# Kernel optimization log

Hardware: AMD Instinct MI355X
Metric: run time of the kernel (lower is better)

The kernel has to match this reference:

```python
import jax, jax.numpy as jnp
import numpy as np

WS = 8      # window size
NH = 8      # num heads
DIM = 192


def _rel_coords_table(ws):
    c = np.arange(-(ws - 1), ws, dtype=np.float32)
    t = np.stack(np.meshgrid(c, c, indexing='ij'), axis=-1)  # (2ws-1, 2ws-1, 2)
    t = t / (ws - 1) * 8.0
    t = np.sign(t) * np.log2(np.abs(t) + 1.0) / np.log2(8.0)
    return jnp.asarray(t.reshape(-1, 2))


def _rel_pos_index(ws):
    coords = np.stack(np.meshgrid(np.arange(ws), np.arange(ws), indexing='ij'))  # (2,ws,ws)
    cf = coords.reshape(2, -1)
    rel = (cf[:, :, None] - cf[:, None, :]).transpose(1, 2, 0).astype(np.int64)  # (N,N,2)
    rel[..., 0] += ws - 1
    rel[..., 1] += ws - 1
    rel[..., 0] *= 2 * ws - 1
    return jnp.asarray(rel.sum(-1))  # (N,N)


_RCT = _rel_coords_table(WS)   # (225, 2)
_RPI = _rel_pos_index(WS)      # (64, 64)


def setup_inputs() -> dict:
    key = jax.random.key(0)
    ks = jax.random.split(key, 6)
    B, C, H, W = 4, DIM, 256, 256
    return {
        'x': jax.random.normal(ks[0], (B, C, H, W), dtype=jnp.float32),
        'img_alpha': jnp.ones((B, 1, H, W), dtype=jnp.float32),
        'qkv_w': jax.random.normal(ks[1], (3 * C, C), dtype=jnp.float32) * 0.02,
        'q_bias': jnp.zeros((C,), dtype=jnp.float32),
        'v_bias': jnp.zeros((C,), dtype=jnp.float32),
        'logit_scale': jnp.full((NH, 1, 1), np.log(10.0), dtype=jnp.float32),
        'cpb_w1': jax.random.normal(ks[2], (2, 512), dtype=jnp.float32) * 0.02,
        'cpb_b1': jnp.zeros((512,), dtype=jnp.float32),
        'cpb_w2': jax.random.normal(ks[3], (512, NH), dtype=jnp.float32) * 0.02,
        'proj_w': jax.random.normal(ks[4], (C, C), dtype=jnp.float32) * 0.02,
        'proj_b': jnp.zeros((C,), dtype=jnp.float32),
    }


def _forward(x, qkv_w, q_bias, v_bias, logit_scale, cpb_w1, cpb_b1, cpb_w2, proj_w, proj_b):
    B, C, H, W = x.shape
    ws, nh = WS, NH
    hd = C // nh
    # window partition: (B,C,H,W) -> (B*nW, N, C) with N = ws*ws
    xw = (x.transpose(0, 2, 3, 1)
           .reshape(B, H // ws, ws, W // ws, ws, C)
           .transpose(0, 1, 3, 2, 4, 5)
           .reshape(-1, ws * ws, C))
    Bw, N, _ = xw.shape
    # qkv with bias = [q_bias, 0, v_bias]
    qkv_b = jnp.concatenate([q_bias, jnp.zeros_like(v_bias), v_bias])
    qkv = (xw @ qkv_w.T + qkv_b).reshape(Bw, N, 3, nh, hd).transpose(2, 0, 3, 1, 4)
    q, k, v = qkv[0], qkv[1], qkv[2]  # (Bw, nh, N, hd)
    # cosine attention with clamped learnable logit scale
    qn = q / jnp.maximum(jnp.linalg.norm(q, axis=-1, keepdims=True), 1e-12)
    kn = k / jnp.maximum(jnp.linalg.norm(k, axis=-1, keepdims=True), 1e-12)
    scale = jnp.exp(jnp.minimum(logit_scale, jnp.log(jnp.float32(100.0))))  # (nh,1,1)
    attn = jnp.einsum('bhnd,bhmd->bhnm', qn, kn) * scale
    # relative position bias from small MLP + gather
    table = jax.nn.relu(_RCT @ cpb_w1 + cpb_b1) @ cpb_w2        # (225, nh)
    bias = table[_RPI.reshape(-1)].reshape(N, N, nh).transpose(2, 0, 1)  # (nh,N,N)
    bias = 16.0 * jax.nn.sigmoid(bias)
    attn = jax.nn.softmax(attn + bias[None], axis=-1)
    out = jnp.einsum('bhnm,bhmd->bhnd', attn, v).transpose(0, 2, 1, 3).reshape(Bw, N, C)
    out = out @ proj_w.T + proj_b
    # window reverse -> (B,C,H,W)
    out = (out.reshape(B, H // ws, W // ws, ws, ws, C)
              .transpose(0, 1, 3, 2, 4, 5)
              .reshape(B, H, W, C)
              .transpose(0, 3, 1, 2))
    return x + out  # residual (shortcut)


def reference(x, img_alpha, qkv_w, q_bias, v_bias, logit_scale,
              cpb_w1, cpb_b1, cpb_w2, proj_w, proj_b):
    # shift_size == 0: img_alpha only rides along through partition and is sliced off;
    # with all-ones alpha the zero-window removal is a no-op, so it does not affect output.
    del img_alpha
    return _forward(x, qkv_w, q_bias, v_bias, logit_scale,
                    cpb_w1, cpb_b1, cpb_w2, proj_w, proj_b)
```

## Files before the change

kernel.cpp:

```cpp
#include <hip/hip_runtime.h>

typedef unsigned short u16;
typedef __attribute__((ext_vector_type(8))) short bf16x8;
typedef __attribute__((ext_vector_type(4))) float f32x4;

#define C_    192
#define HW_   65536

__device__ inline u16 f2bf(float f) {
  union { float f; unsigned u; } x; x.f = f;
  unsigned r = x.u + 0x7FFFu + ((x.u >> 16) & 1u);
  return (u16)(r >> 16);
}
__device__ inline float bf2f(u16 s) {
  union { unsigned u; float f; } x; x.u = ((unsigned)s) << 16;
  return x.f;
}

__global__ void k_convert(const float* __restrict__ qkv_w, const float* __restrict__ proj_w,
                          const float* __restrict__ q_bias, const float* __restrict__ v_bias,
                          u16* __restrict__ wq, u16* __restrict__ wp, float* __restrict__ qkvb) {
  int i = blockIdx.x * 256 + threadIdx.x;
  if (i < 110592) wq[i] = f2bf(qkv_w[i]);
  else if (i < 147456) wp[i - 110592] = f2bf(proj_w[i - 110592]);
  else if (i < 148032) {
    int j = i - 147456;
    qkvb[j] = (j < 192) ? q_bias[j] : ((j < 384) ? 0.f : v_bias[j - 384]);
  }
}

__global__ void k_table(const float* __restrict__ w1, const float* __restrict__ b1,
                        const float* __restrict__ w2, float* __restrict__ table) {
  int row = blockIdx.x;
  int tid = threadIdx.x;
  int a = row / 15, b = row % 15;
  float va = (float)(a - 7) * (8.0f / 7.0f);
  float vb = (float)(b - 7) * (8.0f / 7.0f);
  float c0 = copysignf(log2f(fabsf(va) + 1.0f) * (1.0f / 3.0f), va);
  float c1 = copysignf(log2f(fabsf(vb) + 1.0f) * (1.0f / 3.0f), vb);
  float acc[8];
#pragma unroll
  for (int o = 0; o < 8; ++o) acc[o] = 0.f;
  for (int k = tid; k < 512; k += 256) {
    float h = fmaxf(c0 * w1[k] + c1 * w1[512 + k] + b1[k], 0.f);
#pragma unroll
    for (int o = 0; o < 8; ++o) acc[o] += h * w2[k * 8 + o];
  }
  __shared__ float part[4][8];
  int wave = tid >> 6;
#pragma unroll
  for (int o = 0; o < 8; ++o) {
    float v = acc[o];
    v += __shfl_xor(v, 1, 64);  v += __shfl_xor(v, 2, 64);
    v += __shfl_xor(v, 4, 64);  v += __shfl_xor(v, 8, 64);
    v += __shfl_xor(v, 16, 64); v += __shfl_xor(v, 32, 64);
    acc[o] = v;
  }
  if ((tid & 63) == 0)
#pragma unroll
    for (int o = 0; o < 8; ++o) part[wave][o] = acc[o];
  __syncthreads();
  if (tid < 8)
    table[row * 8 + tid] = part[0][tid] + part[1][tid] + part[2][tid] + part[3][tid];
}

__global__ void k_biasfill(const float* __restrict__ table, float* __restrict__ bias3) {
  int p = blockIdx.x * 256 + threadIdx.x;
  int h = p >> 12, t = (p >> 6) & 63, g = (p >> 4) & 3, u = p & 15;
  int nt = u >> 2, r = u & 3;
  int s = nt * 16 + g * 4 + r;
  int idx = ((t >> 3) - (s >> 3) + 7) * 15 + ((t & 7) - (s & 7) + 7);
  float v = table[idx * 8 + h];
  bias3[p] = 16.0f / (1.0f + __expf(-v));
}

__device__ __forceinline__ void attn_window(
    u16* __restrict__ R0, u16* __restrict__ Sw, float* __restrict__ ikw,
    const u16* __restrict__ wq, const float* __restrict__ qkvb,
    const float* __restrict__ bias3,
    int h, int g, int li, float scaleh,
    const bf16x8* qw0, const bf16x8* qw1) {
  bf16x8 z8 = {0, 0, 0, 0, 0, 0, 0, 0};
  f32x4 zf = {0.f, 0.f, 0.f, 0.f};
  float iqr[4];
  bf16x8 qf[4], kf[4];

  {
    f32x4 cb0 = *(const f32x4*)(qkvb + h * 24 + g * 4);
    f32x4 cb1 = *(const f32x4*)(qkvb + h * 24 + 16 + g * 4);
#pragma unroll
    for (int tb = 0; tb < 4; ++tb) {
      int t = tb * 16 + li;
      bf16x8 xf[6];
#pragma unroll
      for (int ks = 0; ks < 6; ++ks)
        xf[ks] = *(const bf16x8*)&R0[t * 200 + ks * 32 + g * 8];
      f32x4 a0 = zf, a1 = zf;
#pragma unroll
      for (int ks = 0; ks < 6; ++ks) {
        a0 = __builtin_amdgcn_mfma_f32_16x16x32_bf16(qw0[ks], xf[ks], a0, 0, 0, 0);
        a1 = __builtin_amdgcn_mfma_f32_16x16x32_bf16(qw1[ks], xf[ks], a1, 0, 0, 0);
      }
      float p = 0.f;
#pragma unroll
      for (int r = 0; r < 4; ++r) { a0[r] += cb0[r]; p += a0[r] * a0[r]; }
      if (g < 2) {
#pragma unroll
        for (int r = 0; r < 4; ++r) { a1[r] += cb1[r]; p += a1[r] * a1[r]; }
      }
      p += __shfl_xor(p, 16, 64);
      p += __shfl_xor(p, 32, 64);
      iqr[tb] = __builtin_amdgcn_rsqf(fmaxf(p, 1e-24f)) * scaleh;
      uint2 pk;
      pk.x = f2bf(a0[0]) | ((unsigned)f2bf(a0[1]) << 16);
      pk.y = f2bf(a0[2]) | ((unsigned)f2bf(a0[3]) << 16);
      *(uint2*)&Sw[t * 24 + g * 4] = pk;
      if (g < 2) {
        pk.x = f2bf(a1[0]) | ((unsigned)f2bf(a1[1]) << 16);
        pk.y = f2bf(a1[2]) | ((unsigned)f2bf(a1[3]) << 16);
        *(uint2*)&Sw[t * 24 + 16 + g * 4] = pk;
      }
    }
  }

  bf16x8 kw0[6], kw1[6];
  {
    const u16* wr0 = wq + (size_t)(192 + h * 24 + li) * 192 + g * 8;
    const u16* wr1 = wq + (size_t)(192 + h * 24 + 16 + (li & 7)) * 192 + g * 8;
#pragma unroll
    for (int ks = 0; ks < 6; ++ks) {
      kw0[ks] = *(const bf16x8*)(wr0 + ks * 32);
      kw1[ks] = *(const bf16x8*)(wr1 + ks * 32);
    }
  }
#pragma unroll
  for (int tb = 0; tb < 4; ++tb)
    qf[tb] = (g < 3) ? *(const bf16x8*)&Sw[(tb * 16 + li) * 24 + g * 8] : z8;

  {
    f32x4 cb0 = *(const f32x4*)(qkvb + 192 + h * 24 + g * 4);
    f32x4 cb1 = *(const f32x4*)(qkvb + 192 + h * 24 + 16 + g * 4);
#pragma unroll
    for (int nt = 0; nt < 4; ++nt) {
      int t = nt * 16 + li;
      bf16x8 xf[6];
#pragma unroll
      for (int ks = 0; ks < 6; ++ks)
        xf[ks] = *(const bf16x8*)&R0[t * 200 + ks * 32 + g * 8];
      f32x4 a0 = zf, a1 = zf;
#pragma unroll
      for (int ks = 0; ks < 6; ++ks) {
        a0 = __builtin_amdgcn_mfma_f32_16x16x32_bf16(kw0[ks], xf[ks], a0, 0, 0, 0);
        a1 = __builtin_amdgcn_mfma_f32_16x16x32_bf16(kw1[ks], xf[ks], a1, 0, 0, 0);
      }
      float p = 0.f;
#pragma unroll
      for (int r = 0; r < 4; ++r) { a0[r] += cb0[r]; p += a0[r] * a0[r]; }
      if (g < 2) {
#pragma unroll
        for (int r = 0; r < 4; ++r) { a1[r] += cb1[r]; p += a1[r] * a1[r]; }
      }
      p += __shfl_xor(p, 16, 64);
      p += __shfl_xor(p, 32, 64);
      float ik = __builtin_amdgcn_rsqf(fmaxf(p, 1e-24f));
      if (g == 0) ikw[h * 64 + t] = ik;
      uint2 pk;
      pk.x = f2bf(a0[0]) | ((unsigned)f2bf(a0[1]) << 16);
      pk.y = f2bf(a0[2]) | ((unsigned)f2bf(a0[3]) << 16);
      *(uint2*)&Sw[t * 24 + g * 4] = pk;
      if (g < 2) {
        pk.x = f2bf(a1[0]) | ((unsigned)f2bf(a1[1]) << 16);
        pk.y = f2bf(a1[2]) | ((unsigned)f2bf(a1[3]) << 16);
        *(uint2*)&Sw[t * 24 + 16 + g * 4] = pk;
      }
    }
  }

  bf16x8 vw0[6], vw1[6];
  {
    const u16* wr0 = wq + (size_t)(384 + h * 24 + li) * 192 + g * 8;
    const u16* wr1 = wq + (size_t)(384 + h * 24 + 16 + (li & 7)) * 192 + g * 8;
#pragma unroll
    for (int ks = 0; ks < 6; ++ks) {
      vw0[ks] = *(const bf16x8*)(wr0 + ks * 32);
      vw1[ks] = *(const bf16x8*)(wr1 + ks * 32);
    }
  }
#pragma unroll
  for (int nt = 0; nt < 4; ++nt)
    kf[nt] = (g < 3) ? *(const bf16x8*)&Sw[(nt * 16 + li) * 24 + g * 8] : z8;

  {
    float vb0 = qkvb[384 + h * 24 + li];
    float vb1 = qkvb[384 + h * 24 + 16 + (li & 7)];
#pragma unroll
    for (int tb = 0; tb < 4; ++tb) {
      int t = tb * 16 + li;
      bf16x8 xf[6];
#pragma unroll
      for (int ks = 0; ks < 6; ++ks)
        xf[ks] = *(const bf16x8*)&R0[t * 200 + ks * 32 + g * 8];
      f32x4 a0 = zf, a1 = zf;
#pragma unroll
      for (int ks = 0; ks < 6; ++ks) {
        a0 = __builtin_amdgcn_mfma_f32_16x16x32_bf16(xf[ks], vw0[ks], a0, 0, 0, 0);
        a1 = __builtin_amdgcn_mfma_f32_16x16x32_bf16(xf[ks], vw1[ks], a1, 0, 0, 0);
      }
      uint2 pk;
      pk.x = f2bf(a0[0] + vb0) | ((unsigned)f2bf(a0[1] + vb0) << 16);
      pk.y = f2bf(a0[2] + vb0) | ((unsigned)f2bf(a0[3] + vb0) << 16);
      *(uint2*)&Sw[li * 64 + tb * 16 + g * 4] = pk;
      if (li < 8) {
        pk.x = f2bf(a1[0] + vb1) | ((unsigned)f2bf(a1[1] + vb1) << 16);
        pk.y = f2bf(a1[2] + vb1) | ((unsigned)f2bf(a1[3] + vb1) << 16);
        *(uint2*)&Sw[(16 + li) * 64 + tb * 16 + g * 4] = pk;
      }
    }
  }
  bf16x8 vf0[2], vf1[2];
#pragma unroll
  for (int ks = 0; ks < 2; ++ks) {
    vf0[ks] = *(const bf16x8*)&Sw[li * 64 + ks * 32 + g * 8];
    vf1[ks] = (li < 8) ? *(const bf16x8*)&Sw[(16 + li) * 64 + ks * 32 + g * 8] : z8;
  }

  f32x4 bx[2][4];
  {
    const float* bp0 = bias3 + ((h * 64 + li) << 6) + (g << 4);
#pragma unroll
    for (int nt = 0; nt < 4; ++nt) bx[0][nt] = *(const f32x4*)(bp0 + (nt << 2));
  }
#pragma unroll
  for (int tb = 0; tb < 4; ++tb) {
    if (tb < 3) {
      const float* bpn = bias3 + ((h * 64 + (tb + 1) * 16 + li) << 6) + (g << 4);
#pragma unroll
      for (int nt = 0; nt < 4; ++nt) bx[(tb + 1) & 1][nt] = *(const f32x4*)(bpn + (nt << 2));
    }
    f32x4 s4[4];
#pragma unroll
    for (int nt = 0; nt < 4; ++nt)
      s4[nt] = __builtin_amdgcn_mfma_f32_16x16x32_bf16(kf[nt], qf[tb], zf, 0, 0, 0);
    float iq = iqr[tb];
#pragma unroll
    for (int nt = 0; nt < 4; ++nt) {
      f32x4 ik4 = *(const f32x4*)&ikw[h * 64 + nt * 16 + g * 4];
#pragma unroll
      for (int r = 0; r < 4; ++r)
        s4[nt][r] = s4[nt][r] * iq * ik4[r] + bx[tb & 1][nt][r];
    }
    float m = s4[0][0];
#pragma unroll
    for (int nt = 0; nt < 4; ++nt)
#pragma unroll
      for (int r = 0; r < 4; ++r) m = fmaxf(m, s4[nt][r]);
    m = fmaxf(m, __shfl_xor(m, 16, 64));
    m = fmaxf(m, __shfl_xor(m, 32, 64));
    float sum = 0.f;
#pragma unroll
    for (int nt = 0; nt < 4; ++nt)
#pragma unroll
      for (int r = 0; r < 4; ++r) { float e = __expf(s4[nt][r] - m); s4[nt][r] = e; sum += e; }
    sum += __shfl_xor(sum, 16, 64);
    sum += __shfl_xor(sum, 32, 64);
    float is = __builtin_amdgcn_rcpf(sum);
#pragma unroll
    for (int nt = 0; nt < 4; ++nt) {
      uint2 pk;
      pk.x = f2bf(s4[nt][0]) | ((unsigned)f2bf(s4[nt][1]) << 16);
      pk.y = f2bf(s4[nt][2]) | ((unsigned)f2bf(s4[nt][3]) << 16);
      *(uint2*)&Sw[li * 72 + nt * 16 + g * 4] = pk;
    }
    f32x4 o0 = zf, o1 = zf;
#pragma unroll
    for (int ks = 0; ks < 2; ++ks) {
      bf16x8 pf = *(const bf16x8*)&Sw[li * 72 + ks * 32 + g * 8];
      o0 = __builtin_amdgcn_mfma_f32_16x16x32_bf16(vf0[ks], pf, o0, 0, 0, 0);
      o1 = __builtin_amdgcn_mfma_f32_16x16x32_bf16(vf1[ks], pf, o1, 0, 0, 0);
    }
    int t = tb * 16 + li;
    {
      uint2 pk;
      pk.x = f2bf(o0[0] * is) | ((unsigned)f2bf(o0[1] * is) << 16);
      pk.y = f2bf(o0[2] * is) | ((unsigned)f2bf(o0[3] * is) << 16);
      *(uint2*)&R0[t * 200 + h * 24 + g * 4] = pk;
    }
    if (g < 2) {
      uint2 pk;
      pk.x = f2bf(o1[0] * is) | ((unsigned)f2bf(o1[1] * is) << 16);
      pk.y = f2bf(o1[2] * is) | ((unsigned)f2bf(o1[3] * is) << 16);
      *(uint2*)&R0[t * 200 + h * 24 + 16 + g * 4] = pk;
    }
  }
}

__global__ __launch_bounds__(512, 2)
void k_main(const float* __restrict__ x,
            const float* __restrict__ ls, const float* __restrict__ proj_b,
            const u16* __restrict__ wq, const u16* __restrict__ wp,
            const float* __restrict__ qkvb, const float* __restrict__ bias3,
            float* __restrict__ out) {
  __shared__ u16 smem[38912];
  u16* R0A = smem;
  u16* R0B = smem + 12800;
  u16* Sc  = smem + 25600;
  float* ikw = (float*)(smem + 37888);

  int tid  = threadIdx.x;
  int h = tid >> 6, lane = tid & 63, g = lane >> 4, li = lane & 15;
  int tt = h & 3, half = h >> 2;
  int bid = blockIdx.x;
  int b = bid >> 9, rem = bid & 511, wy = rem >> 4, wxp = rem & 15;
  const float* xb = x + (size_t)b * C_ * HW_;
  int baseA = (wy * 8) * 256 + wxp * 16;
  f32x4 zf = {0.f, 0.f, 0.f, 0.f};

  bf16x8 qwA0[6], qwA1[6];
  {
    const u16* wr0 = wq + (size_t)(h * 24 + li) * 192 + g * 8;
    const u16* wr1 = wq + (size_t)(h * 24 + 16 + (li & 7)) * 192 + g * 8;
#pragma unroll
    for (int ks = 0; ks < 6; ++ks) {
      qwA0[ks] = *(const bf16x8*)(wr0 + ks * 32);
      qwA1[ks] = *(const bf16x8*)(wr1 + ks * 32);
    }
  }

#pragma unroll
  for (int it = 0; it < 12; ++it) {
    int i4 = tid + it * 512;
    int c = i4 >> 5, r5 = i4 & 31;
    int ty = r5 >> 2, jq = (r5 & 3) * 4;
    float4 v = *(const float4*)(xb + c * HW_ + baseA + ty * 256 + jq);
    u16* Rw = (jq < 8) ? R0A : R0B;
    int t0 = ty * 8 + (jq & 7);
    Rw[(t0 + 0) * 200 + c] = f2bf(v.x);
    Rw[(t0 + 1) * 200 + c] = f2bf(v.y);
    Rw[(t0 + 2) * 200 + c] = f2bf(v.z);
    Rw[(t0 + 3) * 200 + c] = f2bf(v.w);
  }
  __syncthreads();

  u16* Sw = Sc + h * 1536;
  float scaleh = __expf(fminf(ls[h], 4.6051702f));

  attn_window(R0A, Sw, ikw, wq, qkvb, bias3, h, g, li, scaleh, qwA0, qwA1);

  bf16x8 qwB0[6], qwB1[6];
  {
    const u16* wr0 = wq + (size_t)(h * 24 + li) * 192 + g * 8;
    const u16* wr1 = wq + (size_t)(h * 24 + 16 + (li & 7)) * 192 + g * 8;
#pragma unroll
    for (int ks = 0; ks < 6; ++ks) {
      qwB0[ks] = *(const bf16x8*)(wr0 + ks * 32);
      qwB1[ks] = *(const bf16x8*)(wr1 + ks * 32);
    }
  }
  attn_window(R0B, Sw, ikw, wq, qkvb, bias3, h, g, li, scaleh, qwB0, qwB1);
  __syncthreads();

  bf16x8 afA[6], afB[6];
#pragma unroll
  for (int ks = 0; ks < 6; ++ks) {
    afA[ks] = *(const bf16x8*)&R0A[(tt * 16 + li) * 200 + ks * 32 + g * 8];
    afB[ks] = *(const bf16x8*)&R0B[(tt * 16 + li) * 200 + ks * 32 + g * 8];
  }
  __syncthreads();

  u16* obufA = Sc;
  u16* obufB = smem;
#pragma unroll
  for (int it = 0; it < 6; ++it) {
    int ct = half * 96 + it * 16;
    const u16* wr = wp + (size_t)(ct + li) * 192 + g * 8;
    bf16x8 w6[6];
#pragma unroll
    for (int ks = 0; ks < 6; ++ks) w6[ks] = *(const bf16x8*)(wr + ks * 32);
    f32x4 aA0 = zf, aA1 = zf, aB0 = zf, aB1 = zf;
#pragma unroll
    for (int ks = 0; ks < 3; ++ks) {
      aA0 = __builtin_amdgcn_mfma_f32_16x16x32_bf16(afA[ks], w6[ks], aA0, 0, 0, 0);
      aA1 = __builtin_amdgcn_mfma_f32_16x16x32_bf16(afA[ks + 3], w6[ks + 3], aA1, 0, 0, 0);
      aB0 = __builtin_amdgcn_mfma_f32_16x16x32_bf16(afB[ks], w6[ks], aB0, 0, 0, 0);
      aB1 = __builtin_amdgcn_mfma_f32_16x16x32_bf16(afB[ks + 3], w6[ks + 3], aB1, 0, 0, 0);
    }
    float pb = proj_b[ct + li];
    uint2 pk;
    pk.x = f2bf(aA0[0] + aA1[0] + pb) | ((unsigned)f2bf(aA0[1] + aA1[1] + pb) << 16);
    pk.y = f2bf(aA0[2] + aA1[2] + pb) | ((unsigned)f2bf(aA0[3] + aA1[3] + pb) << 16);
    *(uint2*)&obufA[(ct + li) * 68 + tt * 16 + g * 4] = pk;
    pk.x = f2bf(aB0[0] + aB1[0] + pb) | ((unsigned)f2bf(aB0[1] + aB1[1] + pb) << 16);
    pk.y = f2bf(aB0[2] + aB1[2] + pb) | ((unsigned)f2bf(aB0[3] + aB1[3] + pb) << 16);
    *(uint2*)&obufB[(ct + li) * 68 + tt * 16 + g * 4] = pk;
  }
  __syncthreads();

  float* ob = out + (size_t)b * C_ * HW_;
#pragma unroll
  for (int bt = 0; bt < 2; ++bt) {
    float4 xv[6];
    uint2 ov[6];
#pragma unroll
    for (int it = 0; it < 6; ++it) {
      int i4 = tid + (bt * 6 + it) * 512;
      int c = i4 >> 5, r5 = i4 & 31;
      int ty = r5 >> 2, jq = (r5 & 3) * 4;
      xv[it] = *(const float4*)(xb + c * HW_ + baseA + ty * 256 + jq);
    }
#pragma unroll
    for (int it = 0; it < 6; ++it) {
      int i4 = tid + (bt * 6 + it) * 512;
      int c = i4 >> 5, r5 = i4 & 31;
      int ty = r5 >> 2, jq = (r5 & 3) * 4;
      const u16* obw = (jq < 8) ? obufA : obufB;
      ov[it] = *(const uint2*)&obw[c * 68 + ty * 8 + (jq & 7)];
    }
#pragma unroll
    for (int it = 0; it < 6; ++it) {
      int i4 = tid + (bt * 6 + it) * 512;
      int c = i4 >> 5, r5 = i4 & 31;
      int ty = r5 >> 2, jq = (r5 & 3) * 4;
      float4 r;
      r.x = xv[it].x + bf2f((u16)(ov[it].x & 0xFFFFu));
      r.y = xv[it].y + bf2f((u16)(ov[it].x >> 16));
      r.z = xv[it].z + bf2f((u16)(ov[it].y & 0xFFFFu));
      r.w = xv[it].w + bf2f((u16)(ov[it].y >> 16));
      *(float4*)(ob + c * HW_ + baseA + ty * 256 + jq) = r;
    }
  }
}

extern "C" void kernel_launch(void* const* d_in, const int* in_sizes, int n_in,
                              void* d_out, int out_size, void* d_ws, size_t ws_size,
                              hipStream_t stream) {
  const float* x      = (const float*)d_in[0];
  const float* qkv_w  = (const float*)d_in[2];
  const float* q_bias = (const float*)d_in[3];
  const float* v_bias = (const float*)d_in[4];
  const float* ls     = (const float*)d_in[5];
  const float* w1     = (const float*)d_in[6];
  const float* b1     = (const float*)d_in[7];
  const float* w2     = (const float*)d_in[8];
  const float* proj_w = (const float*)d_in[9];
  const float* proj_b = (const float*)d_in[10];

  u16*   wq    = (u16*)d_ws;
  u16*   wpv   = wq + 110592;
  float* qkvb  = (float*)((char*)d_ws + 294912);
  float* bias3 = (float*)((char*)d_ws + 297216);
  float* table = (float*)((char*)d_ws + 428288);
  float* out   = (float*)d_out;

  hipLaunchKernelGGL(k_convert, dim3(579), dim3(256), 0, stream,
                     qkv_w, proj_w, q_bias, v_bias, wq, wpv, qkvb);
  hipLaunchKernelGGL(k_table, dim3(225), dim3(256), 0, stream, w1, b1, w2, table);
  hipLaunchKernelGGL(k_biasfill, dim3(128), dim3(256), 0, stream, table, bias3);
  hipLaunchKernelGGL(k_main, dim3(2048), dim3(512), 0, stream,
                     x, ls, proj_b, wq, wpv, qkvb, bias3, out);
}
```

Baseline: 424.8 us.

## Process two window pairs per block and pad V scratch stride

Each block now loops over two adjacent window pairs, which halves the grid to 1024 blocks and loads the Q weight fragments into registers once per block instead of twice per pair. The V transpose scratch row stride grows from 64 to 72 elements, likely to cut LDS bank conflicts. The key-norm buffer becomes a separate per-head slice outside the scratch area. The aim is less redundant weight loading and block launch overhead, at the cost of fewer blocks to spread across CUs and slightly more LDS per block.

```diff
diff --git a/kernel.cpp b/kernel.cpp
--- a/kernel.cpp
+++ b/kernel.cpp
@@ -163,7 +163,7 @@
       p += __shfl_xor(p, 16, 64);
       p += __shfl_xor(p, 32, 64);
       float ik = __builtin_amdgcn_rsqf(fmaxf(p, 1e-24f));
-      if (g == 0) ikw[h * 64 + t] = ik;
+      if (g == 0) ikw[t] = ik;
       uint2 pk;
       pk.x = f2bf(a0[0]) | ((unsigned)f2bf(a0[1]) << 16);
       pk.y = f2bf(a0[2]) | ((unsigned)f2bf(a0[3]) << 16);
@@ -209,19 +209,19 @@
       uint2 pk;
       pk.x = f2bf(a0[0] + vb0) | ((unsigned)f2bf(a0[1] + vb0) << 16);
       pk.y = f2bf(a0[2] + vb0) | ((unsigned)f2bf(a0[3] + vb0) << 16);
-      *(uint2*)&Sw[li * 64 + tb * 16 + g * 4] = pk;
+      *(uint2*)&Sw[li * 72 + tb * 16 + g * 4] = pk;
       if (li < 8) {
         pk.x = f2bf(a1[0] + vb1) | ((unsigned)f2bf(a1[1] + vb1) << 16);
         pk.y = f2bf(a1[2] + vb1) | ((unsigned)f2bf(a1[3] + vb1) << 16);
-        *(uint2*)&Sw[(16 + li) * 64 + tb * 16 + g * 4] = pk;
+        *(uint2*)&Sw[(16 + li) * 72 + tb * 16 + g * 4] = pk;
       }
     }
   }
   bf16x8 vf0[2], vf1[2];
 #pragma unroll
   for (int ks = 0; ks < 2; ++ks) {
-    vf0[ks] = *(const bf16x8*)&Sw[li * 64 + ks * 32 + g * 8];
-    vf1[ks] = (li < 8) ? *(const bf16x8*)&Sw[(16 + li) * 64 + ks * 32 + g * 8] : z8;
+    vf0[ks] = *(const bf16x8*)&Sw[li * 72 + ks * 32 + g * 8];
+    vf1[ks] = (li < 8) ? *(const bf16x8*)&Sw[(16 + li) * 72 + ks * 32 + g * 8] : z8;
   }
 
   f32x4 bx[2][4];
@@ -244,7 +244,7 @@
     float iq = iqr[tb];
 #pragma unroll
     for (int nt = 0; nt < 4; ++nt) {
-      f32x4 ik4 = *(const f32x4*)&ikw[h * 64 + nt * 16 + g * 4];
+      f32x4 ik4 = *(const f32x4*)&ikw[nt * 16 + g * 4];
 #pragma unroll
       for (int r = 0; r < 4; ++r)
         s4[nt][r] = s4[nt][r] * iq * ik4[r] + bx[tb & 1][nt][r];
@@ -300,133 +300,127 @@
             const u16* __restrict__ wq, const u16* __restrict__ wp,
             const float* __restrict__ qkvb, const float* __restrict__ bias3,
             float* __restrict__ out) {
-  __shared__ u16 smem[38912];
+  __shared__ u16 smem[40448];
   u16* R0A = smem;
   u16* R0B = smem + 12800;
   u16* Sc  = smem + 25600;
-  float* ikw = (float*)(smem + 37888);
+  float* ikwb = (float*)(smem + 39424);
 
   int tid  = threadIdx.x;
   int h = tid >> 6, lane = tid & 63, g = lane >> 4, li = lane & 15;
   int tt = h & 3, half = h >> 2;
   int bid = blockIdx.x;
-  int b = bid >> 9, rem = bid & 511, wy = rem >> 4, wxp = rem & 15;
+  int b = bid >> 8, rem = bid & 255, wy = rem >> 3, wxq = rem & 7;
   const float* xb = x + (size_t)b * C_ * HW_;
-  int baseA = (wy * 8) * 256 + wxp * 16;
   f32x4 zf = {0.f, 0.f, 0.f, 0.f};
 
-  bf16x8 qwA0[6], qwA1[6];
+  u16* Sw = Sc + h * 1728;
+  float* ikw = ikwb + h * 64;
+  float scaleh = __expf(fminf(ls[h], 4.6051702f));
+
+  bf16x8 qw0[6], qw1[6];
   {
     const u16* wr0 = wq + (size_t)(h * 24 + li) * 192 + g * 8;
     const u16* wr1 = wq + (size_t)(h * 24 + 16 + (li & 7)) * 192 + g * 8;
 #pragma unroll
     for (int ks = 0; ks < 6; ++ks) {
-      qwA0[ks] = *(const bf16x8*)(wr0 + ks * 32);
-      qwA1[ks] = *(const bf16x8*)(wr1 + ks * 32);
-    }
-  }
-
-#pragma unroll
-  for (int it = 0; it < 12; ++it) {
-    int i4 = tid + it * 512;
-    int c = i4 >> 5, r5 = i4 & 31;
-    int ty = r5 >> 2, jq = (r5 & 3) * 4;
-    float4 v = *(const float4*)(xb + c * HW_ + baseA + ty * 256 + jq);
-    u16* Rw = (jq < 8) ? R0A : R0B;
-    int t0 = ty * 8 + (jq & 7);
-    Rw[(t0 + 0) * 200 + c] = f2bf(v.x);
-    Rw[(t0 + 1) * 200 + c] = f2bf(v.y);
-    Rw[(t0 + 2) * 200 + c] = f2bf(v.z);
-    Rw[(t0 + 3) * 200 + c] = f2bf(v.w);
-  }
-  __syncthreads();
-
-  u16* Sw = Sc + h * 1536;
-  float scaleh = __expf(fminf(ls[h], 4.6051702f));
-
-  attn_window(R0A, Sw, ikw, wq, qkvb, bias3, h, g, li, scaleh, qwA0, qwA1);
-
-  bf16x8 qwB0[6], qwB1[6];
-  {
-    const u16* wr0 = wq + (size_t)(h * 24 + li) * 192 + g * 8;
-    const u16* wr1 = wq + (size_t)(h * 24 + 16 + (li & 7)) * 192 + g * 8;
-#pragma unroll
-    for (int ks = 0; ks < 6; ++ks) {
-      qwB0[ks] = *(const bf16x8*)(wr0 + ks * 32);
-      qwB1[ks] = *(const bf16x8*)(wr1 + ks * 32);
-    }
-  }
-  attn_window(R0B, Sw, ikw, wq, qkvb, bias3, h, g, li, scaleh, qwB0, qwB1);
-  __syncthreads();
-
-  bf16x8 afA[6], afB[6];
-#pragma unroll
-  for (int ks = 0; ks < 6; ++ks) {
-    afA[ks] = *(const bf16x8*)&R0A[(tt * 16 + li) * 200 + ks * 32 + g * 8];
-    afB[ks] = *(const bf16x8*)&R0B[(tt * 16 + li) * 200 + ks * 32 + g * 8];
-  }
-  __syncthreads();
-
-  u16* obufA = Sc;
-  u16* obufB = smem;
-#pragma unroll
-  for (int it = 0; it < 6; ++it) {
-    int ct = half * 96 + it * 16;
-    const u16* wr = wp + (size_t)(ct + li) * 192 + g * 8;
-    bf16x8 w6[6];
-#pragma unroll
-    for (int ks = 0; ks < 6; ++ks) w6[ks] = *(const bf16x8*)(wr + ks * 32);
-    f32x4 aA0 = zf, aA1 = zf, aB0 = zf, aB1 = zf;
-#pragma unroll
-    for (int ks = 0; ks < 3; ++ks) {
-      aA0 = __builtin_amdgcn_mfma_f32_16x16x32_bf16(afA[ks], w6[ks], aA0, 0, 0, 0);
-      aA1 = __builtin_amdgcn_mfma_f32_16x16x32_bf16(afA[ks + 3], w6[ks + 3], aA1, 0, 0, 0);
-      aB0 = __builtin_amdgcn_mfma_f32_16x16x32_bf16(afB[ks], w6[ks], aB0, 0, 0, 0);
-      aB1 = __builtin_amdgcn_mfma_f32_16x16x32_bf16(afB[ks + 3], w6[ks + 3], aB1, 0, 0, 0);
-    }
-    float pb = proj_b[ct + li];
-    uint2 pk;
-    pk.x = f2bf(aA0[0] + aA1[0] + pb) | ((unsigned)f2bf(aA0[1] + aA1[1] + pb) << 16);
-    pk.y = f2bf(aA0[2] + aA1[2] + pb) | ((unsigned)f2bf(aA0[3] + aA1[3] + pb) << 16);
-    *(uint2*)&obufA[(ct + li) * 68 + tt * 16 + g * 4] = pk;
-    pk.x = f2bf(aB0[0] + aB1[0] + pb) | ((unsigned)f2bf(aB0[1] + aB1[1] + pb) << 16);
-    pk.y = f2bf(aB0[2] + aB1[2] + pb) | ((unsigned)f2bf(aB0[3] + aB1[3] + pb) << 16);
-    *(uint2*)&obufB[(ct + li) * 68 + tt * 16 + g * 4] = pk;
-  }
-  __syncthreads();
-
-  float* ob = out + (size_t)b * C_ * HW_;
-#pragma unroll
-  for (int bt = 0; bt < 2; ++bt) {
-    float4 xv[6];
-    uint2 ov[6];
-#pragma unroll
-    for (int it = 0; it < 6; ++it) {
-      int i4 = tid + (bt * 6 + it) * 512;
+      qw0[ks] = *(const bf16x8*)(wr0 + ks * 32);
+      qw1[ks] = *(const bf16x8*)(wr1 + ks * 32);
+    }
+  }
+
+  for (int pair = 0; pair < 2; ++pair) {
+    int baseA = (wy * 8) * 256 + wxq * 32 + pair * 16;
+
+#pragma unroll
+    for (int it = 0; it < 12; ++it) {
+      int i4 = tid + it * 512;
       int c = i4 >> 5, r5 = i4 & 31;
       int ty = r5 >> 2, jq = (r5 & 3) * 4;
-      xv[it] = *(const float4*)(xb + c * HW_ + baseA + ty * 256 + jq);
-    }
+      float4 v = *(const float4*)(xb + c * HW_ + baseA + ty * 256 + jq);
+      u16* Rw = (jq < 8) ? R0A : R0B;
+      int t0 = ty * 8 + (jq & 7);
+      Rw[(t0 + 0) * 200 + c] = f2bf(v.x);
+      Rw[(t0 + 1) * 200 + c] = f2bf(v.y);
+      Rw[(t0 + 2) * 200 + c] = f2bf(v.z);
+      Rw[(t0 + 3) * 200 + c] = f2bf(v.w);
+    }
+    __syncthreads();
+
+    attn_window(R0A, Sw, ikw, wq, qkvb, bias3, h, g, li, scaleh, qw0, qw1);
+    attn_window(R0B, Sw, ikw, wq, qkvb, bias3, h, g, li, scaleh, qw0, qw1);
+    __syncthreads();
+
+    bf16x8 afA[6], afB[6];
+#pragma unroll
+    for (int ks = 0; ks < 6; ++ks) {
+      afA[ks] = *(const bf16x8*)&R0A[(tt * 16 + li) * 200 + ks * 32 + g * 8];
+      afB[ks] = *(const bf16x8*)&R0B[(tt * 16 + li) * 200 + ks * 32 + g * 8];
+    }
+    __syncthreads();
+
+    u16* obufA = Sc;
+    u16* obufB = smem;
 #pragma unroll
     for (int it = 0; it < 6; ++it) {
-      int i4 = tid + (bt * 6 + it) * 512;
-      int c = i4 >> 5, r5 = i4 & 31;
-      int ty = r5 >> 2, jq = (r5 & 3) * 4;
-      const u16* obw = (jq < 8) ? obufA : obufB;
-      ov[it] = *(const uint2*)&obw[c * 68 + ty * 8 + (jq & 7)];
-    }
-#pragma unroll
-    for (int it = 0; it < 6; ++it) {
-      int i4 = tid + (bt * 6 + it) * 512;
-      int c = i4 >> 5, r5 = i4 & 31;
-      int ty = r5 >> 2, jq = (r5 & 3) * 4;
-      float4 r;
-      r.x = xv[it].x + bf2f((u16)(ov[it].x & 0xFFFFu));
-      r.y = xv[it].y + bf2f((u16)(ov[it].x >> 16));
-      r.z = xv[it].z + bf2f((u16)(ov[it].y & 0xFFFFu));
-      r.w = xv[it].w + bf2f((u16)(ov[it].y >> 16));
-      *(float4*)(ob + c * HW_ + baseA + ty * 256 + jq) = r;
-    }
+      int ct = half * 96 + it * 16;
+      const u16* wr = wp + (size_t)(ct + li) * 192 + g * 8;
+      bf16x8 w6[6];
+#pragma unroll
+      for (int ks = 0; ks < 6; ++ks) w6[ks] = *(const bf16x8*)(wr + ks * 32);
+      f32x4 aA0 = zf, aA1 = zf, aB0 = zf, aB1 = zf;
+#pragma unroll
+      for (int ks = 0; ks < 3; ++ks) {
+        aA0 = __builtin_amdgcn_mfma_f32_16x16x32_bf16(afA[ks], w6[ks], aA0, 0, 0, 0);
+        aA1 = __builtin_amdgcn_mfma_f32_16x16x32_bf16(afA[ks + 3], w6[ks + 3], aA1, 0, 0, 0);
+        aB0 = __builtin_amdgcn_mfma_f32_16x16x32_bf16(afB[ks], w6[ks], aB0, 0, 0, 0);
+        aB1 = __builtin_amdgcn_mfma_f32_16x16x32_bf16(afB[ks + 3], w6[ks + 3], aB1, 0, 0, 0);
+      }
+      float pb = proj_b[ct + li];
+      uint2 pk;
+      pk.x = f2bf(aA0[0] + aA1[0] + pb) | ((unsigned)f2bf(aA0[1] + aA1[1] + pb) << 16);
+      pk.y = f2bf(aA0[2] + aA1[2] + pb) | ((unsigned)f2bf(aA0[3] + aA1[3] + pb) << 16);
+      *(uint2*)&obufA[(ct + li) * 68 + tt * 16 + g * 4] = pk;
+      pk.x = f2bf(aB0[0] + aB1[0] + pb) | ((unsigned)f2bf(aB0[1] + aB1[1] + pb) << 16);
+      pk.y = f2bf(aB0[2] + aB1[2] + pb) | ((unsigned)f2bf(aB0[3] + aB1[3] + pb) << 16);
+      *(uint2*)&obufB[(ct + li) * 68 + tt * 16 + g * 4] = pk;
+    }
+    __syncthreads();
+
+    float* ob = out + (size_t)b * C_ * HW_;
+#pragma unroll
+    for (int bt = 0; bt < 2; ++bt) {
+      float4 xv[6];
+      uint2 ov[6];
+#pragma unroll
+      for (int it = 0; it < 6; ++it) {
+        int i4 = tid + (bt * 6 + it) * 512;
+        int c = i4 >> 5, r5 = i4 & 31;
+        int ty = r5 >> 2, jq = (r5 & 3) * 4;
+        xv[it] = *(const float4*)(xb + c * HW_ + baseA + ty * 256 + jq);
+      }
+#pragma unroll
+      for (int it = 0; it < 6; ++it) {
+        int i4 = tid + (bt * 6 + it) * 512;
+        int c = i4 >> 5, r5 = i4 & 31;
+        int ty = r5 >> 2, jq = (r5 & 3) * 4;
+        const u16* obw = (jq < 8) ? obufA : obufB;
+        ov[it] = *(const uint2*)&obw[c * 68 + ty * 8 + (jq & 7)];
+      }
+#pragma unroll
+      for (int it = 0; it < 6; ++it) {
+        int i4 = tid + (bt * 6 + it) * 512;
+        int c = i4 >> 5, r5 = i4 & 31;
+        int ty = r5 >> 2, jq = (r5 & 3) * 4;
+        float4 r;
+        r.x = xv[it].x + bf2f((u16)(ov[it].x & 0xFFFFu));
+        r.y = xv[it].y + bf2f((u16)(ov[it].x >> 16));
+        r.z = xv[it].z + bf2f((u16)(ov[it].y & 0xFFFFu));
+        r.w = xv[it].w + bf2f((u16)(ov[it].y >> 16));
+        *(float4*)(ob + c * HW_ + baseA + ty * 256 + jq) = r;
+      }
+    }
+    if (pair == 0) __syncthreads();
   }
 }
 
@@ -455,6 +449,6 @@
                      qkv_w, proj_w, q_bias, v_bias, wq, wpv, qkvb);
   hipLaunchKernelGGL(k_table, dim3(225), dim3(256), 0, stream, w1, b1, w2, table);
   hipLaunchKernelGGL(k_biasfill, dim3(128), dim3(256), 0, stream, table, bias3);
-  hipLaunchKernelGGL(k_main, dim3(2048), dim3(512), 0, stream,
+  hipLaunchKernelGGL(k_main, dim3(1024), dim3(512), 0, stream,
                      x, ls, proj_b, wq, wpv, qkvb, bias3, out);
 }
```

Result: slower. 1.422 ms (+234.8%).

## Process four windows per 1024-thread block and pad V tile stride

Applied to the files above, without the earlier changes.

Each block of k_main now handles four adjacent 8x8 windows with 16 waves instead of two windows with 8 waves. Each row is loaded as a 32-float segment, so global loads and stores are wider and better coalesced. Scratch space and ikw buffers are now per wave, and the V tile row stride is padded from 64 to 72 to reduce LDS bank conflicts. The cost is that LDS use roughly doubles to about 158 KB, which allows only one block per CU. The new launch bounds (1024, 4) also ask for much higher occupancy than that LDS use permits, which may force a low VGPR cap and cause register spills.

```diff
diff --git a/kernel.cpp b/kernel.cpp
--- a/kernel.cpp
+++ b/kernel.cpp
@@ -163,7 +163,7 @@
       p += __shfl_xor(p, 16, 64);
       p += __shfl_xor(p, 32, 64);
       float ik = __builtin_amdgcn_rsqf(fmaxf(p, 1e-24f));
-      if (g == 0) ikw[h * 64 + t] = ik;
+      if (g == 0) ikw[t] = ik;
       uint2 pk;
       pk.x = f2bf(a0[0]) | ((unsigned)f2bf(a0[1]) << 16);
       pk.y = f2bf(a0[2]) | ((unsigned)f2bf(a0[3]) << 16);
@@ -209,19 +209,19 @@
       uint2 pk;
       pk.x = f2bf(a0[0] + vb0) | ((unsigned)f2bf(a0[1] + vb0) << 16);
       pk.y = f2bf(a0[2] + vb0) | ((unsigned)f2bf(a0[3] + vb0) << 16);
-      *(uint2*)&Sw[li * 64 + tb * 16 + g * 4] = pk;
+      *(uint2*)&Sw[li * 72 + tb * 16 + g * 4] = pk;
       if (li < 8) {
         pk.x = f2bf(a1[0] + vb1) | ((unsigned)f2bf(a1[1] + vb1) << 16);
         pk.y = f2bf(a1[2] + vb1) | ((unsigned)f2bf(a1[3] + vb1) << 16);
-        *(uint2*)&Sw[(16 + li) * 64 + tb * 16 + g * 4] = pk;
+        *(uint2*)&Sw[(16 + li) * 72 + tb * 16 + g * 4] = pk;
       }
     }
   }
   bf16x8 vf0[2], vf1[2];
 #pragma unroll
   for (int ks = 0; ks < 2; ++ks) {
-    vf0[ks] = *(const bf16x8*)&Sw[li * 64 + ks * 32 + g * 8];
-    vf1[ks] = (li < 8) ? *(const bf16x8*)&Sw[(16 + li) * 64 + ks * 32 + g * 8] : z8;
+    vf0[ks] = *(const bf16x8*)&Sw[li * 72 + ks * 32 + g * 8];
+    vf1[ks] = (li < 8) ? *(const bf16x8*)&Sw[(16 + li) * 72 + ks * 32 + g * 8] : z8;
   }
 
   f32x4 bx[2][4];
@@ -244,7 +244,7 @@
     float iq = iqr[tb];
 #pragma unroll
     for (int nt = 0; nt < 4; ++nt) {
-      f32x4 ik4 = *(const f32x4*)&ikw[h * 64 + nt * 16 + g * 4];
+      f32x4 ik4 = *(const f32x4*)&ikw[nt * 16 + g * 4];
 #pragma unroll
       for (int r = 0; r < 4; ++r)
         s4[nt][r] = s4[nt][r] * iq * ik4[r] + bx[tb & 1][nt][r];
@@ -294,26 +294,29 @@
   }
 }
 
-__global__ __launch_bounds__(512, 2)
+__global__ __launch_bounds__(1024, 4)
 void k_main(const float* __restrict__ x,
             const float* __restrict__ ls, const float* __restrict__ proj_b,
             const u16* __restrict__ wq, const u16* __restrict__ wp,
             const float* __restrict__ qkvb, const float* __restrict__ bias3,
             float* __restrict__ out) {
-  __shared__ u16 smem[38912];
-  u16* R0A = smem;
-  u16* R0B = smem + 12800;
-  u16* Sc  = smem + 25600;
-  float* ikw = (float*)(smem + 37888);
+  __shared__ u16 smem[80896];
+  u16* Sc = smem + 51200;
+  float* ikwb = (float*)(smem + 78848);
 
   int tid  = threadIdx.x;
-  int h = tid >> 6, lane = tid & 63, g = lane >> 4, li = lane & 15;
-  int tt = h & 3, half = h >> 2;
+  int w = tid >> 6, lane = tid & 63, g = lane >> 4, li = lane & 15;
+  int h = w & 7, pr = w >> 3;
+  int tt = w & 3, half = (w >> 2) & 1;
   int bid = blockIdx.x;
-  int b = bid >> 9, rem = bid & 511, wy = rem >> 4, wxp = rem & 15;
+  int b = bid >> 8, rem = bid & 255, wy = rem >> 3, wxq = rem & 7;
   const float* xb = x + (size_t)b * C_ * HW_;
-  int baseA = (wy * 8) * 256 + wxp * 16;
+  int base = (wy * 8) * 256 + wxq * 32;
   f32x4 zf = {0.f, 0.f, 0.f, 0.f};
+
+  u16* Sw = Sc + w * 1728;
+  float* ikw = ikwb + w * 64;
+  float scaleh = __expf(fminf(ls[h], 4.6051702f));
 
   bf16x8 qwA0[6], qwA1[6];
   {
@@ -328,11 +331,11 @@
 
 #pragma unroll
   for (int it = 0; it < 12; ++it) {
-    int i4 = tid + it * 512;
-    int c = i4 >> 5, r5 = i4 & 31;
-    int ty = r5 >> 2, jq = (r5 & 3) * 4;
-    float4 v = *(const float4*)(xb + c * HW_ + baseA + ty * 256 + jq);
-    u16* Rw = (jq < 8) ? R0A : R0B;
+    int i4 = tid + it * 1024;
+    int c = i4 >> 6, r6 = i4 & 63;
+    int ty = r6 >> 3, jq = (r6 & 7) * 4;
+    float4 v = *(const float4*)(xb + c * HW_ + base + ty * 256 + jq);
+    u16* Rw = smem + (jq >> 3) * 12800;
     int t0 = ty * 8 + (jq & 7);
     Rw[(t0 + 0) * 200 + c] = f2bf(v.x);
     Rw[(t0 + 1) * 200 + c] = f2bf(v.y);
@@ -341,11 +344,9 @@
   }
   __syncthreads();
 
-  u16* Sw = Sc + h * 1536;
-  float scaleh = __expf(fminf(ls[h], 4.6051702f));
-
+  u16* R0A = smem + (pr * 2) * 12800;
+  u16* R0B = smem + (pr * 2 + 1) * 12800;
   attn_window(R0A, Sw, ikw, wq, qkvb, bias3, h, g, li, scaleh, qwA0, qwA1);
-
   bf16x8 qwB0[6], qwB1[6];
   {
     const u16* wr0 = wq + (size_t)(h * 24 + li) * 192 + g * 8;
@@ -367,8 +368,8 @@
   }
   __syncthreads();
 
-  u16* obufA = Sc;
-  u16* obufB = smem;
+  u16* obufA = smem + (pr * 2) * 13056;
+  u16* obufB = smem + (pr * 2 + 1) * 13056;
 #pragma unroll
   for (int it = 0; it < 6; ++it) {
     int ct = half * 96 + it * 16;
@@ -402,30 +403,30 @@
     uint2 ov[6];
 #pragma unroll
     for (int it = 0; it < 6; ++it) {
-      int i4 = tid + (bt * 6 + it) * 512;
-      int c = i4 >> 5, r5 = i4 & 31;
-      int ty = r5 >> 2, jq = (r5 & 3) * 4;
-      xv[it] = *(const float4*)(xb + c * HW_ + baseA + ty * 256 + jq);
+      int i4 = tid + (bt * 6 + it) * 1024;
+      int c = i4 >> 6, r6 = i4 & 63;
+      int ty = r6 >> 3, jq = (r6 & 7) * 4;
+      xv[it] = *(const float4*)(xb + c * HW_ + base + ty * 256 + jq);
     }
 #pragma unroll
     for (int it = 0; it < 6; ++it) {
-      int i4 = tid + (bt * 6 + it) * 512;
-      int c = i4 >> 5, r5 = i4 & 31;
-      int ty = r5 >> 2, jq = (r5 & 3) * 4;
-      const u16* obw = (jq < 8) ? obufA : obufB;
+      int i4 = tid + (bt * 6 + it) * 1024;
+      int c = i4 >> 6, r6 = i4 & 63;
+      int ty = r6 >> 3, jq = (r6 & 7) * 4;
+      const u16* obw = smem + (jq >> 3) * 13056;
       ov[it] = *(const uint2*)&obw[c * 68 + ty * 8 + (jq & 7)];
     }
 #pragma unroll
     for (int it = 0; it < 6; ++it) {
-      int i4 = tid + (bt * 6 + it) * 512;
-      int c = i4 >> 5, r5 = i4 & 31;
-      int ty = r5 >> 2, jq = (r5 & 3) * 4;
+      int i4 = tid + (bt * 6 + it) * 1024;
+      int c = i4 >> 6, r6 = i4 & 63;
+      int ty = r6 >> 3, jq = (r6 & 7) * 4;
       float4 r;
       r.x = xv[it].x + bf2f((u16)(ov[it].x & 0xFFFFu));
       r.y = xv[it].y + bf2f((u16)(ov[it].x >> 16));
       r.z = xv[it].z + bf2f((u16)(ov[it].y & 0xFFFFu));
       r.w = xv[it].w + bf2f((u16)(ov[it].y >> 16));
-      *(float4*)(ob + c * HW_ + baseA + ty * 256 + jq) = r;
+      *(float4*)(ob + c * HW_ + base + ty * 256 + jq) = r;
     }
   }
 }
@@ -455,6 +456,6 @@
                      qkv_w, proj_w, q_bias, v_bias, wq, wpv, qkvb);
   hipLaunchKernelGGL(k_table, dim3(225), dim3(256), 0, stream, w1, b1, w2, table);
   hipLaunchKernelGGL(k_biasfill, dim3(128), dim3(256), 0, stream, table, bias3);
-  hipLaunchKernelGGL(k_main, dim3(2048), dim3(512), 0, stream,
+  hipLaunchKernelGGL(k_main, dim3(1024), dim3(1024), 0, stream,
                      x, ls, proj_b, wq, wpv, qkvb, bias3, out);
 }
```

Result: slower. 779.0 us (+83.4%).
